# Kernel optimization log

Hardware: AMD Instinct MI355X
Metric: run time of the kernel (lower is better)

The kernel has to match this reference:

```python
import jax, jax.numpy as jnp
import numpy as np

EMB = 1024
HEADS = 16
HEADSIZE = EMB // HEADS
EPS = 1e-5  # torch LayerNorm default


def _layernorm(x, g, b):
    # normalize over last dim (headsize)
    m = jnp.mean(x, axis=-1, keepdims=True)
    v = jnp.mean((x - m) ** 2, axis=-1, keepdims=True)
    return (x - m) * jax.lax.rsqrt(v + EPS) * g + b


def setup_inputs() -> dict:
    key = jax.random.key(0)
    ks = jax.random.split(key, 6)
    B, T = 4, 2048
    s = 1.0 / np.sqrt(EMB)  # ~ torch Linear init scale
    return {
        "x": jax.random.normal(ks[0], (B, T, EMB), dtype=jnp.float32),
        "Wk": jax.random.normal(ks[1], (EMB, EMB), dtype=jnp.float32) * s,
        "Wq": jax.random.normal(ks[2], (EMB, EMB), dtype=jnp.float32) * s,
        "Wv": jax.random.normal(ks[3], (EMB, EMB), dtype=jnp.float32) * s,
        "Wo": jax.random.normal(ks[4], (EMB, EMB), dtype=jnp.float32) * s,
        "bo": jnp.zeros((EMB,), dtype=jnp.float32),
        "kln_g": jnp.ones((HEADSIZE,), dtype=jnp.float32),
        "kln_b": jnp.zeros((HEADSIZE,), dtype=jnp.float32),
        "qln_g": jnp.ones((HEADSIZE,), dtype=jnp.float32),
        "qln_b": jnp.zeros((HEADSIZE,), dtype=jnp.float32),
    }


def reference(x, Wk, Wq, Wv, Wo, bo, kln_g, kln_b, qln_g, qln_b):
    B, T, E = x.shape
    # projections (torch Linear: y = x @ W.T), split into heads
    k = jnp.einsum("bte,fe->btf", x, Wk).reshape(B, T, HEADS, HEADSIZE)
    q = jnp.einsum("bte,fe->btf", x, Wq).reshape(B, T, HEADS, HEADSIZE)
    v = jnp.einsum("bte,fe->btf", x, Wv).reshape(B, T, HEADS, HEADSIZE)
    # optional per-head layernorm on keys/queries (kqnorm=True)
    k = _layernorm(k, kln_g, kln_b)
    q = _layernorm(q, qln_g, qln_b)
    # note: original scales by emb**-1/4 on each of q and k (total 1/sqrt(emb))
    scale = E ** (-0.25)
    q = q * scale
    k = k * scale
    # full [B, H, T, T] score matrix (faithful to bmm implementation)
    dot = jnp.einsum("bihd,bjhd->bhij", q, k)
    # causal mask: j > i set to -inf (mask_diagonal=False -> offset=1)
    causal = jnp.triu(jnp.ones((T, T), dtype=bool), k=1)
    dot = jnp.where(causal, -jnp.inf, dot)
    att = jax.nn.softmax(dot, axis=-1)
    out = jnp.einsum("bhij,bjhd->bihd", att, v).reshape(B, T, E)
    return jnp.einsum("bte,fe->btf", out, Wo) + bo
```

## Files before the change

### kernel.cpp

```cpp
#include <hip/hip_runtime.h>
#include <hip/hip_bf16.h>
#include <cstdint>

#define EMB 1024
#define HEADS 16
#define HD 64
#define BATCH 4
#define SEQ 2048
#define BT (BATCH*SEQ)
#define LNEPS 1e-5f
#define QK_SCALE 0.17677669529663687f
#define LOG2E 1.4426950408889634f

typedef __bf16 bf16;
typedef __bf16 bf16x8 __attribute__((ext_vector_type(8)));
typedef __bf16 bf16x4 __attribute__((ext_vector_type(4)));
typedef float  f32x4  __attribute__((ext_vector_type(4)));
typedef short  s16x4  __attribute__((ext_vector_type(4)));

typedef const __attribute__((address_space(1))) void* gas_ptr;
typedef __attribute__((address_space(3))) void*       las_ptr;

__device__ __forceinline__ void gld_lds16(const void* g, void* l) {
  __builtin_amdgcn_global_load_lds((gas_ptr)g, (las_ptr)l, 16, 0, 0);
}

__device__ __forceinline__ f32x4 mfma_pv(bf16x4 a, bf16x4 b, f32x4 c) {
  return __builtin_amdgcn_mfma_f32_16x16x16bf16_1k(
      __builtin_bit_cast(s16x4, a), __builtin_bit_cast(s16x4, b), c, 0, 0, 0);
}

__global__ void cvt_all(const float* __restrict__ x,
                        const float* __restrict__ w0, const float* __restrict__ w1,
                        const float* __restrict__ w2, const float* __restrict__ w3,
                        bf16* __restrict__ xb, bf16* __restrict__ wb) {
  const int bid = blockIdx.x;
  if (bid < 8192) {
    int i = bid * 256 + threadIdx.x;
    float4 f = reinterpret_cast<const float4*>(x)[i];
    bf16x4 o = { (bf16)f.x, (bf16)f.y, (bf16)f.z, (bf16)f.w };
    reinterpret_cast<bf16x4*>(xb)[i] = o;
  } else {
    int i = (bid - 8192) * 256 + threadIdx.x;
    int sel = i >> 18;
    int j = i & 262143;
    const float* s = (sel == 0) ? w0 : (sel == 1) ? w1 : (sel == 2) ? w2 : w3;
    float4 f = reinterpret_cast<const float4*>(s)[j];
    bf16x4 o = { (bf16)f.x, (bf16)f.y, (bf16)f.z, (bf16)f.w };
    reinterpret_cast<bf16x4*>(wb)[i] = o;
  }
}

#define GEMM_DBUF_LOOP(A_, B_, K_)                                            \
  f32x4 zero4 = {0.f, 0.f, 0.f, 0.f};                                         \
  f32x4 acc[4][4];                                                            \
  _Pragma("unroll")                                                           \
  for (int i = 0; i < 4; i++)                                                 \
    _Pragma("unroll")                                                         \
    for (int j = 0; j < 4; j++) acc[i][j] = zero4;                            \
  const int u0_ = t * 8, u1_ = t * 8 + 2048;                                  \
  const int sr0 = u0_ >> 5, sc0 = ((t & 3) ^ ((sr0 >> 1) & 3));               \
  const int sr1 = u1_ >> 5, sc1 = ((t & 3) ^ ((sr1 >> 1) & 3));               \
  const int nt_ = K_ / 32;                                                    \
  {                                                                           \
    gld_lds16(A_ + (size_t)(m0 + sr0) * K_ + sc0 * 8, &As[0][u0_]);           \
    gld_lds16(A_ + (size_t)(m0 + sr1) * K_ + sc1 * 8, &As[0][u1_]);           \
    gld_lds16(B_ + (size_t)(n0 + sr0) * K_ + sc0 * 8, &Bs[0][u0_]);           \
    gld_lds16(B_ + (size_t)(n0 + sr1) * K_ + sc1 * 8, &Bs[0][u1_]);           \
  }                                                                           \
  for (int kt = 0; kt < nt_; ++kt) {                                          \
    const int buf = kt & 1;                                                   \
    __syncthreads();                                                          \
    if (kt + 1 < nt_) {                                                       \
      const int k0 = (kt + 1) * 32;                                           \
      gld_lds16(A_ + (size_t)(m0 + sr0) * K_ + k0 + sc0 * 8, &As[buf^1][u0_]);\
      gld_lds16(A_ + (size_t)(m0 + sr1) * K_ + k0 + sc1 * 8, &As[buf^1][u1_]);\
      gld_lds16(B_ + (size_t)(n0 + sr0) * K_ + k0 + sc0 * 8, &Bs[buf^1][u0_]);\
      gld_lds16(B_ + (size_t)(n0 + sr1) * K_ + k0 + sc1 * 8, &Bs[buf^1][u1_]);\
    }                                                                         \
    bf16x8 af[4], bfr[4];                                                     \
    _Pragma("unroll")                                                         \
    for (int mi = 0; mi < 4; mi++) {                                          \
      const int row = wm + mi * 16 + ln;                                      \
      af[mi] = *reinterpret_cast<const bf16x8*>(                              \
          &As[buf][row * 32 + ((q ^ ((row >> 1) & 3))) * 8]);                 \
    }                                                                         \
    _Pragma("unroll")                                                         \
    for (int ni = 0; ni < 4; ni++) {                                          \
      const int row = wn + ni * 16 + ln;                                      \
      bfr[ni] = *reinterpret_cast<const bf16x8*>(                             \
          &Bs[buf][row * 32 + ((q ^ ((row >> 1) & 3))) * 8]);                 \
    }                                                                         \
    _Pragma("unroll")                                                         \
    for (int mi = 0; mi < 4; mi++)                                            \
      _Pragma("unroll")                                                       \
      for (int ni = 0; ni < 4; ni++)                                          \
        acc[mi][ni] = __builtin_amdgcn_mfma_f32_16x16x32_bf16(                \
            af[mi], bfr[ni], acc[mi][ni], 0, 0, 0);                           \
  }

__global__ __launch_bounds__(256, 2) void gemm_kqv(
    const bf16* __restrict__ A, const bf16* __restrict__ Bm,
    bf16* __restrict__ kn, bf16* __restrict__ qn, bf16* __restrict__ vt,
    const float* __restrict__ kg, const float* __restrict__ kb,
    const float* __restrict__ qg, const float* __restrict__ qb)
{
  __shared__ __align__(16) bf16 As[2][128 * 32];
  __shared__ __align__(16) bf16 Bs[2][128 * 32];

  const int t    = threadIdx.x;
  const int lane = t & 63;
  const int wave = t >> 6;
  const int q    = lane >> 4;
  const int ln   = lane & 15;

  const int lid = (int)blockIdx.y * (int)gridDim.x + (int)blockIdx.x;
  const int xcd = lid & 7;
  const int nn  = lid >> 3;
  const int bxr = nn >> 3;
  const int byr = (xcd << 3) | (nn & 7);
  const int m0  = byr * 128;
  const int n0  = bxr * 128;

  const int wm = (wave >> 1) * 64;
  const int wn = (wave & 1) * 64;

  GEMM_DBUF_LOOP(A, Bm, EMB)

  const int sec = n0 >> 10;
  const int cb  = (n0 & 1023) + wn;
  const int h   = cb >> 6;
  const int R0  = m0 + wm;

  if (sec == 2) {
#pragma unroll
    for (int mi = 0; mi < 4; mi++) {
      const int R = R0 + mi * 16 + q * 4;
      const int b = R >> 11, tt = R & 2047;
#pragma unroll
      for (int ni = 0; ni < 4; ni++) {
        const int d = ni * 16 + ln;
        bf16x4 o4 = { (bf16)acc[mi][ni][0], (bf16)acc[mi][ni][1],
                      (bf16)acc[mi][ni][2], (bf16)acc[mi][ni][3] };
        *reinterpret_cast<bf16x4*>(
            &vt[((size_t)(b * HEADS + h) * HD + d) * SEQ + tt]) = o4;
      }
    }
  } else {
    const float scale = sec ? QK_SCALE : (QK_SCALE * LOG2E);
    const float* gp = sec ? qg : kg;
    const float* bp = sec ? qb : kb;
    bf16* outp = sec ? qn : kn;
    float gv[4], bv[4];
#pragma unroll
    for (int ni = 0; ni < 4; ni++) {
      gv[ni] = gp[ni * 16 + ln];
      bv[ni] = bp[ni * 16 + ln] * scale;
    }
#pragma unroll
    for (int mi = 0; mi < 4; mi++) {
#pragma unroll
      for (int r = 0; r < 4; r++) {
        const float x0 = acc[mi][0][r], x1 = acc[mi][1][r];
        const float x2 = acc[mi][2][r], x3 = acc[mi][3][r];
        float s  = (x0 + x1) + (x2 + x3);
        float s2 = (x0 * x0 + x1 * x1) + (x2 * x2 + x3 * x3);
#pragma unroll
        for (int mm = 1; mm < 16; mm <<= 1) {
          s  += __shfl_xor(s,  mm, 64);
          s2 += __shfl_xor(s2, mm, 64);
        }
        const float mean = s * (1.f / 64.f);
        const float rs = rsqrtf(s2 * (1.f / 64.f) - mean * mean + LNEPS) * scale;
        const int R = R0 + mi * 16 + q * 4 + r;
        const int b = R >> 11, tt = R & 2047;
        const size_t o = ((size_t)(b * HEADS + h) * SEQ + tt) * HD + ln;
#pragma unroll
        for (int ni = 0; ni < 4; ni++)
          outp[o + ni * 16] = (bf16)((acc[mi][ni][r] - mean) * rs * gv[ni] + bv[ni]);
      }
    }
  }
}

__global__ __launch_bounds__(256, 2) void gemm_out(
    const bf16* __restrict__ A, const bf16* __restrict__ Bm,
    float* __restrict__ Cf, const float* __restrict__ bias, int N)
{
  __shared__ __align__(16) bf16 As[2][128 * 32];
  __shared__ __align__(16) bf16 Bs[2][128 * 32];

  const int t    = threadIdx.x;
  const int lane = t & 63;
  const int wave = t >> 6;
  const int q    = lane >> 4;
  const int ln   = lane & 15;

  const int lid = (int)blockIdx.y * (int)gridDim.x + (int)blockIdx.x;
  const int xcd = lid & 7;
  const int nn  = lid >> 3;
  const int bxr = nn >> 3;
  const int byr = (xcd << 3) | (nn & 7);
  const int m0  = byr * 128;
  const int n0  = bxr * 128;

  const int wm = (wave >> 1) * 64;
  const int wn = (wave & 1) * 64;

  GEMM_DBUF_LOOP(A, Bm, EMB)

#pragma unroll
  for (int mi = 0; mi < 4; mi++) {
#pragma unroll
    for (int ni = 0; ni < 4; ni++) {
#pragma unroll
      for (int r = 0; r < 4; r++) {
        int row = m0 + wm + mi * 16 + q * 4 + r;
        int col = n0 + wn + ni * 16 + ln;
        Cf[(size_t)row * N + col] = acc[mi][ni][r] + bias[col];
      }
    }
  }
}

__global__ __launch_bounds__(256, 4) void attn(
    const bf16* __restrict__ Qn, const bf16* __restrict__ Kn, const bf16* __restrict__ Vt,
    bf16* __restrict__ O)
{
  __shared__ __align__(16) bf16 Ks[2][64 * 64];
  __shared__ __align__(16) bf16 Vs[2][64 * 64];

  const int id = blockIdx.x;
  const int bh = ((id >> 7) << 3) | (id & 7);
  const int bxi = (id >> 3) & 15;
  const int t = threadIdx.x, wave = t >> 6, lane = t & 63;
  const int q = lane >> 4, ln = lane & 15;
  const int b = bh >> 4, h = bh & 15;

  const int u0 = t * 8, u1 = t * 8 + 2048;
  const int kr0 = u0 >> 6, kc0 = ((u0 >> 3) & 7) ^ (kr0 & 7);
  const int kr1 = u1 >> 6, kc1 = ((u1 >> 3) & 7) ^ (kr1 & 7);
  const int vd0 = u0 >> 6, vc0 = ((u0 >> 3) & 7) ^ (vd0 & 7);
  const int vd1 = u1 >> 6, vc1 = ((u1 >> 3) & 7) ^ (vd1 & 7);
  const bf16* Kb = Kn + (size_t)bh * SEQ * HD;
  const bf16* Vb = Vt + (size_t)bh * HD * SEQ;

  f32x4 zero4 = {0.f, 0.f, 0.f, 0.f};

  for (int pass = 0; pass < 2; ++pass) {
    const int itile = pass ? (31 - bxi) : bxi;
    const int qbase = itile * 64 + wave * 16;

    const bf16* qp = Qn + ((size_t)bh * SEQ + qbase + ln) * HD + q * 8;
    bf16x8 qf0 = *reinterpret_cast<const bf16x8*>(qp);
    bf16x8 qf1 = *reinterpret_cast<const bf16x8*>(qp + 32);

    float lrow = 0.f;
    f32x4 oacc[4];
#pragma unroll
    for (int md = 0; md < 4; md++) oacc[md] = zero4;

    const int nj = itile + 1;

    __syncthreads();
    {
      gld_lds16(Kb + (size_t)kr0 * HD + kc0 * 8, &Ks[0][u0]);
      gld_lds16(Kb + (size_t)kr1 * HD + kc1 * 8, &Ks[0][u1]);
      gld_lds16(Vb + (size_t)vd0 * SEQ + vc0 * 8, &Vs[0][u0]);
      gld_lds16(Vb + (size_t)vd1 * SEQ + vc1 * 8, &Vs[0][u1]);
    }

    for (int jt = 0; jt < nj; ++jt) {
      const int buf = jt & 1;
      const int j0 = jt * 64;
      __syncthreads();
      if (jt + 1 < nj) {
        const int jn = j0 + 64;
        gld_lds16(Kb + (size_t)(jn + kr0) * HD + kc0 * 8, &Ks[buf ^ 1][u0]);
        gld_lds16(Kb + (size_t)(jn + kr1) * HD + kc1 * 8, &Ks[buf ^ 1][u1]);
        gld_lds16(Vb + (size_t)vd0 * SEQ + jn + vc0 * 8, &Vs[buf ^ 1][u0]);
        gld_lds16(Vb + (size_t)vd1 * SEQ + jn + vc1 * 8, &Vs[buf ^ 1][u1]);
      }

#pragma unroll
      for (int jb = 0; jb < 4; ++jb) {
        const int jslab = j0 + jb * 16;
        if (jslab <= qbase + 15) {
          const int rowj = jb * 16 + ln;
          bf16x8 kf0 = *reinterpret_cast<const bf16x8*>(
              &Ks[buf][rowj * 64 + ((q)     ^ (rowj & 7)) * 8]);
          bf16x8 kf1 = *reinterpret_cast<const bf16x8*>(
              &Ks[buf][rowj * 64 + ((4 + q) ^ (rowj & 7)) * 8]);
          f32x4 z = zero4;
          z = __builtin_amdgcn_mfma_f32_16x16x32_bf16(kf0, qf0, z, 0, 0, 0);
          z = __builtin_amdgcn_mfma_f32_16x16x32_bf16(kf1, qf1, z, 0, 0, 0);
          if (jslab + 15 > qbase) {
#pragma unroll
            for (int r = 0; r < 4; r++) {
              int jj = jslab + q * 4 + r;
              int ii = qbase + ln;
              if (jj > ii) z[r] = -1.0e30f;
            }
          }
          float p0 = exp2f(z[0]), p1 = exp2f(z[1]), p2 = exp2f(z[2]), p3 = exp2f(z[3]);
          lrow += (p0 + p1) + (p2 + p3);
          bf16x4 pk = { (bf16)p0, (bf16)p1, (bf16)p2, (bf16)p3 };

#pragma unroll
          for (int md = 0; md < 4; md++) {
            const int rowd = md * 16 + ln;
            const bf16* vp = &Vs[buf][rowd * 64 +
                (((jb * 2 + (q >> 1)) ^ (rowd & 7)) * 8) + (q & 1) * 4];
            bf16x4 vf = *reinterpret_cast<const bf16x4*>(vp);
            oacc[md] = mfma_pv(vf, pk, oacc[md]);
          }
        }
      }
    }

    float s = lrow;
    s += __shfl_xor(s, 16, 64);
    s += __shfl_xor(s, 32, 64);
    const float inv = 1.f / s;
    const int row = qbase + ln;
#pragma unroll
    for (int md = 0; md < 4; md++) {
      bf16x4 o4 = { (bf16)(oacc[md][0] * inv), (bf16)(oacc[md][1] * inv),
                    (bf16)(oacc[md][2] * inv), (bf16)(oacc[md][3] * inv) };
      int col = h * HD + md * 16 + q * 4;
      *reinterpret_cast<bf16x4*>(&O[(size_t)(b * SEQ + row) * EMB + col]) = o4;
    }
  }
}

extern "C" void kernel_launch(void* const* d_in, const int* in_sizes, int n_in,
                              void* d_out, int out_size, void* d_ws, size_t ws_size,
                              hipStream_t stream)
{
  const float* x   = (const float*)d_in[0];
  const float* Wk  = (const float*)d_in[1];
  const float* Wq  = (const float*)d_in[2];
  const float* Wv  = (const float*)d_in[3];
  const float* Wo  = (const float*)d_in[4];
  const float* bo  = (const float*)d_in[5];
  const float* klg = (const float*)d_in[6];
  const float* klb = (const float*)d_in[7];
  const float* qlg = (const float*)d_in[8];
  const float* qlb = (const float*)d_in[9];
  float* out = (float*)d_out;

  char* ws = (char*)d_ws;
  const size_t OFF_XB  = 0;
  const size_t OFF_WB  = OFF_XB  + (size_t)BT * EMB * 2;
  const size_t OFF_KQV = OFF_WB  + (size_t)4 * EMB * EMB * 2;
  const size_t OFF_KN  = OFF_KQV + (size_t)BT * 3 * EMB * 2;
  const size_t OFF_QN  = OFF_KN  + (size_t)BT * EMB * 2;
  const size_t OFF_VT  = OFF_QN  + (size_t)BT * EMB * 2;
  const size_t OFF_END = OFF_VT  + (size_t)BT * EMB * 2;
  if (ws_size < OFF_END) return;

  bf16* xb   = (bf16*)(ws + OFF_XB);
  bf16* wb   = (bf16*)(ws + OFF_WB);
  bf16* kn   = (bf16*)(ws + OFF_KN);
  bf16* qn   = (bf16*)(ws + OFF_QN);
  bf16* vt   = (bf16*)(ws + OFF_VT);
  bf16* ob   = (bf16*)(ws + OFF_KQV);

  cvt_all<<<12288, 256, 0, stream>>>(x, Wk, Wq, Wv, Wo, xb, wb);

  gemm_kqv<<<dim3(3 * EMB / 128, BT / 128), 256, 0, stream>>>(
      xb, wb, kn, qn, vt, klg, klb, qlg, qlb);

  attn<<<dim3(16 * BATCH * HEADS), 256, 0, stream>>>(qn, kn, vt, ob);

  gemm_out<<<dim3(EMB / 128, BT / 128), 256, 0, stream>>>(
      ob, wb + (size_t)3 * EMB * EMB, out, bo, EMB);
}
```

Measured before the change: 269.1 us.

## Rewrite output GEMM with 512 threads, K-tile 64, XOR-swizzled LDS

The output projection GEMM now uses 8 waves per block, each computing a 64x32 sub-tile, instead of 4 waves at 64x64. Its K tile doubles from 32 to 64 with an XOR swizzle over 8 column chunks, which halves the number of loop iterations and barriers. The aim is more waves to hide latency and fewer synchronisations per block. In exchange, LDS use doubles to 64KB per block, so fewer blocks can be resident on a CU at once.

After: 267.1 us. Within noise of the previous version (-0.7%).

```diff
diff --git a/kernel.cpp b/kernel.cpp
--- a/kernel.cpp
+++ b/kernel.cpp
@@ -51,7 +51,7 @@
   }
 }
 
-#define GEMM_DBUF_LOOP(A_, B_, K_)                                            \
+#define GEMM_DBUF_LOOP32(A_, B_, K_)                                          \
   f32x4 zero4 = {0.f, 0.f, 0.f, 0.f};                                         \
   f32x4 acc[4][4];                                                            \
   _Pragma("unroll")                                                           \
@@ -125,7 +125,7 @@
   const int wm = (wave >> 1) * 64;
   const int wn = (wave & 1) * 64;
 
-  GEMM_DBUF_LOOP(A, Bm, EMB)
+  GEMM_DBUF_LOOP32(A, Bm, EMB)
 
   const int sec = n0 >> 10;
   const int cb  = (n0 & 1023) + wn;
@@ -183,12 +183,12 @@
   }
 }
 
-__global__ __launch_bounds__(256, 2) void gemm_out(
+__global__ __launch_bounds__(512, 4) void gemm_out(
     const bf16* __restrict__ A, const bf16* __restrict__ Bm,
     float* __restrict__ Cf, const float* __restrict__ bias, int N)
 {
-  __shared__ __align__(16) bf16 As[2][128 * 32];
-  __shared__ __align__(16) bf16 Bs[2][128 * 32];
+  __shared__ __align__(16) bf16 As[2][128 * 64];
+  __shared__ __align__(16) bf16 Bs[2][128 * 64];
 
   const int t    = threadIdx.x;
   const int lane = t & 63;
@@ -204,15 +204,66 @@
   const int m0  = byr * 128;
   const int n0  = bxr * 128;
 
-  const int wm = (wave >> 1) * 64;
-  const int wn = (wave & 1) * 64;
-
-  GEMM_DBUF_LOOP(A, Bm, EMB)
+  const int wm = (wave >> 2) * 64;
+  const int wn = (wave & 3) * 32;
+
+  const int K = EMB;
+  f32x4 zero4 = {0.f, 0.f, 0.f, 0.f};
+  f32x4 acc[4][2];
+#pragma unroll
+  for (int i = 0; i < 4; i++)
+#pragma unroll
+    for (int j = 0; j < 2; j++) acc[i][j] = zero4;
+
+  const int uA0 = t * 8, uA1 = t * 8 + 4096;
+  const int r0_ = uA0 >> 6, c0_ = ((uA0 >> 3) & 7) ^ (r0_ & 7);
+  const int r1_ = uA1 >> 6, c1_ = ((uA1 >> 3) & 7) ^ (r1_ & 7);
+
+  {
+    gld_lds16(A  + (size_t)(m0 + r0_) * K + c0_ * 8, &As[0][uA0]);
+    gld_lds16(A  + (size_t)(m0 + r1_) * K + c1_ * 8, &As[0][uA1]);
+    gld_lds16(Bm + (size_t)(n0 + r0_) * K + c0_ * 8, &Bs[0][uA0]);
+    gld_lds16(Bm + (size_t)(n0 + r1_) * K + c1_ * 8, &Bs[0][uA1]);
+  }
+
+  for (int kt = 0; kt < K / 64; ++kt) {
+    const int buf = kt & 1;
+    __syncthreads();
+    if (kt + 1 < K / 64) {
+      const int k0 = (kt + 1) * 64;
+      gld_lds16(A  + (size_t)(m0 + r0_) * K + k0 + c0_ * 8, &As[buf ^ 1][uA0]);
+      gld_lds16(A  + (size_t)(m0 + r1_) * K + k0 + c1_ * 8, &As[buf ^ 1][uA1]);
+      gld_lds16(Bm + (size_t)(n0 + r0_) * K + k0 + c0_ * 8, &Bs[buf ^ 1][uA0]);
+      gld_lds16(Bm + (size_t)(n0 + r1_) * K + k0 + c1_ * 8, &Bs[buf ^ 1][uA1]);
+    }
+#pragma unroll
+    for (int ks = 0; ks < 2; ++ks) {
+      bf16x8 af[4], bfr[2];
+#pragma unroll
+      for (int mi = 0; mi < 4; mi++) {
+        const int row = wm + mi * 16 + ln;
+        af[mi] = *reinterpret_cast<const bf16x8*>(
+            &As[buf][row * 64 + ((ks * 4 + q) ^ (row & 7)) * 8]);
+      }
+#pragma unroll
+      for (int ni = 0; ni < 2; ni++) {
+        const int row = wn + ni * 16 + ln;
+        bfr[ni] = *reinterpret_cast<const bf16x8*>(
+            &Bs[buf][row * 64 + ((ks * 4 + q) ^ (row & 7)) * 8]);
+      }
+#pragma unroll
+      for (int mi = 0; mi < 4; mi++)
+#pragma unroll
+        for (int ni = 0; ni < 2; ni++)
+          acc[mi][ni] = __builtin_amdgcn_mfma_f32_16x16x32_bf16(
+              af[mi], bfr[ni], acc[mi][ni], 0, 0, 0);
+    }
+  }
 
 #pragma unroll
   for (int mi = 0; mi < 4; mi++) {
 #pragma unroll
-    for (int ni = 0; ni < 4; ni++) {
+    for (int ni = 0; ni < 2; ni++) {
 #pragma unroll
       for (int r = 0; r < 4; r++) {
         int row = m0 + wm + mi * 16 + q * 4 + r;
@@ -373,6 +424,6 @@
 
   attn<<<dim3(16 * BATCH * HEADS), 256, 0, stream>>>(qn, kn, vt, ob);
 
-  gemm_out<<<dim3(EMB / 128, BT / 128), 256, 0, stream>>>(
+  gemm_out<<<dim3(EMB / 128, BT / 128), 512, 0, stream>>>(
       ob, wb + (size_t)3 * EMB * EMB, out, bo, EMB);
 }
```

## Use 128-row attention tiles with 512 threads and 64x128 output GEMM tiles

Applied to the files above, without the earlier changes.

The attention kernel now launches 512-thread blocks that each cover 128 query rows across 8 waves. Each K/V tile loaded into LDS is shared by twice as many query rows, so the grid is halved. The output GEMM switches from 128x128 to 64x128 tiles with its own loop and a remapped 1D grid of 1024 blocks, raising block count and occupancy for this small GEMM. The cost is more redundant B-matrix loads in the GEMM and coarser causal load balancing in attention.

Result: no change. 272.7 us (+1.3%).

```diff
diff --git a/kernel.cpp b/kernel.cpp
--- a/kernel.cpp
+++ b/kernel.cpp
@@ -51,7 +51,7 @@
   }
 }
 
-#define GEMM_DBUF_LOOP(A_, B_, K_)                                            \
+#define GEMM_DBUF_LOOP32(A_, B_, K_)                                          \
   f32x4 zero4 = {0.f, 0.f, 0.f, 0.f};                                         \
   f32x4 acc[4][4];                                                            \
   _Pragma("unroll")                                                           \
@@ -125,7 +125,7 @@
   const int wm = (wave >> 1) * 64;
   const int wn = (wave & 1) * 64;
 
-  GEMM_DBUF_LOOP(A, Bm, EMB)
+  GEMM_DBUF_LOOP32(A, Bm, EMB)
 
   const int sec = n0 >> 10;
   const int cb  = (n0 & 1023) + wn;
@@ -183,11 +183,11 @@
   }
 }
 
-__global__ __launch_bounds__(256, 2) void gemm_out(
+__global__ __launch_bounds__(256, 4) void gemm_out(
     const bf16* __restrict__ A, const bf16* __restrict__ Bm,
     float* __restrict__ Cf, const float* __restrict__ bias, int N)
 {
-  __shared__ __align__(16) bf16 As[2][128 * 32];
+  __shared__ __align__(16) bf16 As[2][64 * 32];
   __shared__ __align__(16) bf16 Bs[2][128 * 32];
 
   const int t    = threadIdx.x;
@@ -196,21 +196,67 @@
   const int q    = lane >> 4;
   const int ln   = lane & 15;
 
-  const int lid = (int)blockIdx.y * (int)gridDim.x + (int)blockIdx.x;
-  const int xcd = lid & 7;
-  const int nn  = lid >> 3;
-  const int bxr = nn >> 3;
-  const int byr = (xcd << 3) | (nn & 7);
-  const int m0  = byr * 128;
-  const int n0  = bxr * 128;
-
-  const int wm = (wave >> 1) * 64;
+  const int id  = blockIdx.x;
+  const int xcd = id & 7;
+  const int nn  = id >> 3;
+  const int n0  = (nn >> 4) * 128;
+  const int m0  = ((xcd << 4) | (nn & 15)) * 64;
+
+  const int wm = (wave >> 1) * 32;
   const int wn = (wave & 1) * 64;
 
-  GEMM_DBUF_LOOP(A, Bm, EMB)
-
-#pragma unroll
-  for (int mi = 0; mi < 4; mi++) {
+  const int K = EMB;
+  f32x4 zero4 = {0.f, 0.f, 0.f, 0.f};
+  f32x4 acc[2][4];
+#pragma unroll
+  for (int i = 0; i < 2; i++)
+#pragma unroll
+    for (int j = 0; j < 4; j++) acc[i][j] = zero4;
+
+  const int ua  = t * 8;
+  const int ra  = ua >> 5, ca = (t & 3) ^ ((ra >> 1) & 3);
+  const int ub0 = t * 8, ub1 = t * 8 + 2048;
+  const int rb0 = ub0 >> 5, cb0 = (t & 3) ^ ((rb0 >> 1) & 3);
+  const int rb1 = ub1 >> 5, cb1 = (t & 3) ^ ((rb1 >> 1) & 3);
+
+  {
+    gld_lds16(A  + (size_t)(m0 + ra)  * K + ca  * 8, &As[0][ua]);
+    gld_lds16(Bm + (size_t)(n0 + rb0) * K + cb0 * 8, &Bs[0][ub0]);
+    gld_lds16(Bm + (size_t)(n0 + rb1) * K + cb1 * 8, &Bs[0][ub1]);
+  }
+
+  for (int kt = 0; kt < K / 32; ++kt) {
+    const int buf = kt & 1;
+    __syncthreads();
+    if (kt + 1 < K / 32) {
+      const int k0 = (kt + 1) * 32;
+      gld_lds16(A  + (size_t)(m0 + ra)  * K + k0 + ca  * 8, &As[buf ^ 1][ua]);
+      gld_lds16(Bm + (size_t)(n0 + rb0) * K + k0 + cb0 * 8, &Bs[buf ^ 1][ub0]);
+      gld_lds16(Bm + (size_t)(n0 + rb1) * K + k0 + cb1 * 8, &Bs[buf ^ 1][ub1]);
+    }
+    bf16x8 af[2], bfr[4];
+#pragma unroll
+    for (int mi = 0; mi < 2; mi++) {
+      const int row = wm + mi * 16 + ln;
+      af[mi] = *reinterpret_cast<const bf16x8*>(
+          &As[buf][row * 32 + ((q ^ ((row >> 1) & 3))) * 8]);
+    }
+#pragma unroll
+    for (int ni = 0; ni < 4; ni++) {
+      const int row = wn + ni * 16 + ln;
+      bfr[ni] = *reinterpret_cast<const bf16x8*>(
+          &Bs[buf][row * 32 + ((q ^ ((row >> 1) & 3))) * 8]);
+    }
+#pragma unroll
+    for (int mi = 0; mi < 2; mi++)
+#pragma unroll
+      for (int ni = 0; ni < 4; ni++)
+        acc[mi][ni] = __builtin_amdgcn_mfma_f32_16x16x32_bf16(
+            af[mi], bfr[ni], acc[mi][ni], 0, 0, 0);
+  }
+
+#pragma unroll
+  for (int mi = 0; mi < 2; mi++) {
 #pragma unroll
     for (int ni = 0; ni < 4; ni++) {
 #pragma unroll
@@ -223,7 +269,7 @@
   }
 }
 
-__global__ __launch_bounds__(256, 4) void attn(
+__global__ __launch_bounds__(512, 4) void attn(
     const bf16* __restrict__ Qn, const bf16* __restrict__ Kn, const bf16* __restrict__ Vt,
     bf16* __restrict__ O)
 {
@@ -231,25 +277,24 @@
   __shared__ __align__(16) bf16 Vs[2][64 * 64];
 
   const int id = blockIdx.x;
-  const int bh = ((id >> 7) << 3) | (id & 7);
-  const int bxi = (id >> 3) & 15;
+  const int xcd = id & 7;
+  const int bxi = (id >> 3) & 7;
+  const int bh  = ((id >> 6) << 3) | xcd;
   const int t = threadIdx.x, wave = t >> 6, lane = t & 63;
   const int q = lane >> 4, ln = lane & 15;
   const int b = bh >> 4, h = bh & 15;
 
-  const int u0 = t * 8, u1 = t * 8 + 2048;
+  const int u0 = t * 8;
   const int kr0 = u0 >> 6, kc0 = ((u0 >> 3) & 7) ^ (kr0 & 7);
-  const int kr1 = u1 >> 6, kc1 = ((u1 >> 3) & 7) ^ (kr1 & 7);
   const int vd0 = u0 >> 6, vc0 = ((u0 >> 3) & 7) ^ (vd0 & 7);
-  const int vd1 = u1 >> 6, vc1 = ((u1 >> 3) & 7) ^ (vd1 & 7);
   const bf16* Kb = Kn + (size_t)bh * SEQ * HD;
   const bf16* Vb = Vt + (size_t)bh * HD * SEQ;
 
   f32x4 zero4 = {0.f, 0.f, 0.f, 0.f};
 
   for (int pass = 0; pass < 2; ++pass) {
-    const int itile = pass ? (31 - bxi) : bxi;
-    const int qbase = itile * 64 + wave * 16;
+    const int itile = pass ? (15 - bxi) : bxi;
+    const int qbase = itile * 128 + wave * 16;
 
     const bf16* qp = Qn + ((size_t)bh * SEQ + qbase + ln) * HD + q * 8;
     bf16x8 qf0 = *reinterpret_cast<const bf16x8*>(qp);
@@ -260,14 +305,12 @@
 #pragma unroll
     for (int md = 0; md < 4; md++) oacc[md] = zero4;
 
-    const int nj = itile + 1;
+    const int nj = 2 * itile + 2;
 
     __syncthreads();
     {
       gld_lds16(Kb + (size_t)kr0 * HD + kc0 * 8, &Ks[0][u0]);
-      gld_lds16(Kb + (size_t)kr1 * HD + kc1 * 8, &Ks[0][u1]);
       gld_lds16(Vb + (size_t)vd0 * SEQ + vc0 * 8, &Vs[0][u0]);
-      gld_lds16(Vb + (size_t)vd1 * SEQ + vc1 * 8, &Vs[0][u1]);
     }
 
     for (int jt = 0; jt < nj; ++jt) {
@@ -277,9 +320,7 @@
       if (jt + 1 < nj) {
         const int jn = j0 + 64;
         gld_lds16(Kb + (size_t)(jn + kr0) * HD + kc0 * 8, &Ks[buf ^ 1][u0]);
-        gld_lds16(Kb + (size_t)(jn + kr1) * HD + kc1 * 8, &Ks[buf ^ 1][u1]);
         gld_lds16(Vb + (size_t)vd0 * SEQ + jn + vc0 * 8, &Vs[buf ^ 1][u0]);
-        gld_lds16(Vb + (size_t)vd1 * SEQ + jn + vc1 * 8, &Vs[buf ^ 1][u1]);
       }
 
 #pragma unroll
@@ -371,8 +412,8 @@
   gemm_kqv<<<dim3(3 * EMB / 128, BT / 128), 256, 0, stream>>>(
       xb, wb, kn, qn, vt, klg, klb, qlg, qlb);
 
-  attn<<<dim3(16 * BATCH * HEADS), 256, 0, stream>>>(qn, kn, vt, ob);
-
-  gemm_out<<<dim3(EMB / 128, BT / 128), 256, 0, stream>>>(
+  attn<<<dim3(8 * BATCH * HEADS), 512, 0, stream>>>(qn, kn, vt, ob);
+
+  gemm_out<<<dim3(1024), 256, 0, stream>>>(
       ob, wb + (size_t)3 * EMB * EMB, out, bo, EMB);
 }
```
